# Kernel optimization log

Measured on AMD Instinct MI355X. Metric: run time of the kernel, lower is better.

Reference implementation:

```python
import jax, jax.numpy as jnp
import numpy as np

ALPHA = 0.1
BETA = 1.1
NUM_CLASSES = 16
EPS = 1e-8  # matches torch cosine_similarity eps
BATCH = 131072
DIM = 512


def setup_inputs() -> dict:
    key = jax.random.key(0)
    k1, k2 = jax.random.split(key)
    embeddings = jax.random.normal(k1, (BATCH, DIM), dtype=jnp.float32)
    labels = jax.random.randint(k2, (BATCH,), 0, NUM_CLASSES)
    return {"embeddings": embeddings, "labels": labels}


def _cos_dist(a, b):
    # a: [M, D], b: [N, D] -> 1 - cosine_similarity, shape [M, N]
    an = a / jnp.maximum(jnp.linalg.norm(a, axis=-1, keepdims=True), EPS)
    bn = b / jnp.maximum(jnp.linalg.norm(b, axis=-1, keepdims=True), EPS)
    return 1.0 - an @ bn.T


def reference(embeddings, labels):
    C = NUM_CLASSES
    N = embeddings.shape[0]
    dt = embeddings.dtype

    # class centroids (dummy anchors) via scatter-mean
    cnt = jax.ops.segment_sum(jnp.ones((N,), dt), labels, num_segments=C)  # [C]
    sums = jax.ops.segment_sum(embeddings, labels, num_segments=C)        # [C, D]
    centroids = sums / jnp.maximum(cnt, 1.0)[:, None]
    present = cnt > 0

    # close class pairs: i < j, both present, centroid distance <= beta
    pd = _cos_dist(centroids, centroids)                    # [C, C]
    upper = jnp.triu(jnp.ones((C, C), bool), k=1)
    pairmask = upper & (pd <= BETA) & present[:, None] & present[None, :]
    pm = pairmask.astype(dt)
    deg = pm.sum(1) + pm.sum(0)                             # pairs involving each class

    # distances from every centroid to every sample
    D = _cos_dist(centroids, embeddings)                    # [C, N]

    # intra: each sample of class c contributes relu(d(cent_c, x) - alpha),
    # once per close pair involving c
    d_own = D[labels, jnp.arange(N)]                        # [N]
    intra_sum = jnp.sum(deg[labels] * jax.nn.relu(d_own - ALPHA))

    # inter: S[c, c'] = sum over samples with label c' of relu(beta - d(cent_c, x))
    S = jax.ops.segment_sum(jax.nn.relu(BETA - D).T, labels, num_segments=C).T  # [C, C]
    inter_sum = jnp.sum(pm * (S + S.T))

    # number of terms in each loss list: sum over pairs of (cnt_i + cnt_j)
    count = jnp.sum(deg * cnt)
    denom = jnp.maximum(count, 1.0)
    num_pairs = pm.sum()

    loss = jnp.where(num_pairs > 0, intra_sum / denom + inter_sum / denom, 0.0)
    return loss
```

## Files before the change

### kernel.cpp

```cpp
#include <hip/hip_runtime.h>

constexpr float kAlpha = 0.1f;
constexpr float kBeta  = 1.1f;
constexpr int   kC     = 16;
constexpr int   kD     = 512;
constexpr float kEps   = 1e-8f;

constexpr int SUMS_OFF = 0;
constexpr int CNT_OFF  = 8192;
constexpr int TOT_OFF  = 8208;
constexpr int CN_OFF   = 8224;
constexpr int MSK_OFF  = 16416;
constexpr int SCL_OFF  = 16432;
constexpr int ZERO_FLOATS = 8209;

__device__ __forceinline__ float dot4(float4 a, float4 b) {
    return a.x * b.x + a.y * b.y + a.z * b.z + a.w * b.w;
}
__device__ __forceinline__ void add4(float4& a, float4 b) {
    a.x += b.x; a.y += b.y; a.z += b.z; a.w += b.w;
}

__global__ __launch_bounds__(256) void k1_sums(const float* __restrict__ emb,
                                               const int* __restrict__ labels,
                                               float* __restrict__ sums,
                                               float* __restrict__ cnt,
                                               int N, int rpb) {
    __shared__ float lacc[kC * kD];
    __shared__ float lcnt[kC];
    int tid = threadIdx.x;
    int wave = tid >> 6, lane = tid & 63;

    for (int i = tid; i < kC * kD; i += 256) lacc[i] = 0.f;
    if (tid < kC) lcnt[tid] = 0.f;

    float4 accA[kC], accB[kC];
#pragma unroll
    for (int c = 0; c < kC; ++c) {
        accA[c] = make_float4(0.f, 0.f, 0.f, 0.f);
        accB[c] = make_float4(0.f, 0.f, 0.f, 0.f);
    }
    float cacc = 0.f;

    const float4* e4 = (const float4*)emb;
    int r0 = blockIdx.x * rpb;
    int r1 = min(r0 + rpb, N);

#define ACC1(c) { add4(accA[c], a0); add4(accB[c], a1); }
#define DO_SWITCH(l)                                                        \
    switch (l) {                                                            \
        case 0:  ACC1(0);  break; case 1:  ACC1(1);  break;                 \
        case 2:  ACC1(2);  break; case 3:  ACC1(3);  break;                 \
        case 4:  ACC1(4);  break; case 5:  ACC1(5);  break;                 \
        case 6:  ACC1(6);  break; case 7:  ACC1(7);  break;                 \
        case 8:  ACC1(8);  break; case 9:  ACC1(9);  break;                 \
        case 10: ACC1(10); break; case 11: ACC1(11); break;                 \
        case 12: ACC1(12); break; case 13: ACC1(13); break;                 \
        case 14: ACC1(14); break; default: ACC1(15); break;                 \
    }

    int r = r0 + wave;
    bool v = (r < r1);
    int rc = v ? r : 0;
    float4 a0 = e4[(size_t)rc * 128 + lane];
    float4 a1 = e4[(size_t)rc * 128 + 64 + lane];
    int la = labels[rc];

    while (v) {
        int rn = r + 4;
        bool vn = (rn < r1);
        int rcn = vn ? rn : 0;
        float4 b0 = e4[(size_t)rcn * 128 + lane];
        float4 b1 = e4[(size_t)rcn * 128 + 64 + lane];
        int lb = labels[rcn];

        int l = __builtin_amdgcn_readfirstlane(la);
        DO_SWITCH(l);
        cacc += (lane < kC && l == lane) ? 1.f : 0.f;

        a0 = b0; a1 = b1; la = lb;
        r = rn; v = vn;
    }
#undef DO_SWITCH
#undef ACC1

    __syncthreads();
#pragma unroll
    for (int c = 0; c < kC; ++c) {
        float* pA = &lacc[c * kD + 4 * lane];
        atomicAdd(pA + 0, accA[c].x);
        atomicAdd(pA + 1, accA[c].y);
        atomicAdd(pA + 2, accA[c].z);
        atomicAdd(pA + 3, accA[c].w);
        float* pB = &lacc[c * kD + 256 + 4 * lane];
        atomicAdd(pB + 0, accB[c].x);
        atomicAdd(pB + 1, accB[c].y);
        atomicAdd(pB + 2, accB[c].z);
        atomicAdd(pB + 3, accB[c].w);
    }
    if (lane < kC) atomicAdd(&lcnt[lane], cacc);
    __syncthreads();
    for (int i = tid; i < kC * kD; i += 256) atomicAdd(&sums[i], lacc[i]);
    if (tid < kC) atomicAdd(&cnt[tid], lcnt[tid]);
}

__global__ __launch_bounds__(256) void k2_cent(const float* __restrict__ sums,
                                               const float* __restrict__ cnt_g,
                                               float* __restrict__ cn_g,
                                               unsigned* __restrict__ mask_g,
                                               float* __restrict__ scal) {
    __shared__ __align__(16) float lcn[kC * kD];
    __shared__ float lcnt[kC];
    __shared__ float red[256];
    __shared__ float norms[kC];
    __shared__ float pdm[kC * kC];
    int tid = threadIdx.x;
    if (tid < kC) lcnt[tid] = cnt_g[tid];
    __syncthreads();

    int c = tid >> 4, sub = tid & 15;
    float invc = 1.f / fmaxf(lcnt[c], 1.f);
    float sq = 0.f;
    for (int d = sub; d < kD; d += 16) {
        float v = sums[c * kD + d] * invc;
        lcn[c * kD + d] = v;
        sq += v * v;
    }
    red[tid] = sq;
    __syncthreads();
    if (tid < kC) {
        float t = 0.f;
        for (int k = 0; k < 16; ++k) t += red[tid * 16 + k];
        norms[tid] = fmaxf(sqrtf(t), kEps);
    }
    __syncthreads();
    for (int i = tid; i < kC * kD; i += 256) {
        float v = lcn[i] / norms[i / kD];
        lcn[i] = v;
        cn_g[i] = v;
    }
    __syncthreads();
    int pi = tid >> 4, pj = tid & 15;
    float dot = 0.f;
    for (int dd = 0; dd < kD; ++dd) {
        int d = (dd + tid) & (kD - 1);
        dot += lcn[pi * kD + d] * lcn[pj * kD + d];
    }
    pdm[tid] = 1.f - dot;
    __syncthreads();
    if (tid == 0) {
        unsigned m[kC];
        for (int a = 0; a < kC; ++a) m[a] = 0u;
        float npairs = 0.f;
        for (int a = 0; a < kC; ++a)
            for (int b = a + 1; b < kC; ++b) {
                bool close = (pdm[a * kC + b] <= kBeta) && (lcnt[a] > 0.f) && (lcnt[b] > 0.f);
                if (close) { m[a] |= 1u << b; m[b] |= 1u << a; npairs += 1.f; }
            }
        float count = 0.f;
        for (int a = 0; a < kC; ++a) {
            mask_g[a] = m[a];
            count += (float)__popc(m[a]) * lcnt[a];
        }
        scal[0] = fmaxf(count, 1.f);
        scal[1] = npairs;
    }
}

constexpr int TR = 32;
__global__ __launch_bounds__(512, 2) void k3_main(const float* __restrict__ emb,
                                                  const int* __restrict__ labels,
                                                  const float* __restrict__ cn_g,
                                                  const unsigned* __restrict__ mask_g,
                                                  float* __restrict__ total,
                                                  int N, int rpb) {
    __shared__ __align__(16) float4 xbuf[TR * 128];
    __shared__ unsigned lmask[kC];
    __shared__ float wsum[8];
    int tid = threadIdx.x;
    int wave = tid >> 6, lane = tid & 63;
    int g = lane >> 4, j = lane & 15;

    const float4* w4 = (const float4*)cn_g;
    float4 wreg[4][8];
#pragma unroll
    for (int c = 0; c < 4; ++c)
#pragma unroll
        for (int i = 0; i < 8; ++i)
            wreg[c][i] = w4[(4 * g + c) * 128 + i * 16 + j];
    if (tid < kC) lmask[tid] = mask_g[tid];

    int r0 = blockIdx.x * rpb;
    int r1 = min(r0 + rpb, N);
    float priv = 0.f;

    const float4* src = (const float4*)emb;
    float4 st[8];

    if (r0 < r1) {
        int avail = (r1 - r0) * 128;
#pragma unroll
        for (int k = 0; k < 8; ++k) {
            int idx = k * 512 + tid;
            st[k] = (idx < avail) ? src[(size_t)r0 * 128 + idx] : make_float4(0.f, 0.f, 0.f, 0.f);
        }
#pragma unroll
        for (int k = 0; k < 8; ++k) xbuf[k * 512 + tid] = st[k];
    }
    __syncthreads();

    for (int rt = r0; rt < r1; rt += TR) {
        int ntile = rt + TR;
        bool more = (ntile < r1);
        if (more) {
            int avail = (r1 - ntile) * 128;
#pragma unroll
            for (int k = 0; k < 8; ++k) {
                int idx = k * 512 + tid;
                st[k] = (idx < avail) ? src[(size_t)ntile * 128 + idx] : make_float4(0.f, 0.f, 0.f, 0.f);
            }
        }

        int rows = min(TR, r1 - rt);
        for (int rr = wave; rr < rows; rr += 8) {
            int row = rt + rr;
            int lab = labels[row];
            const float4* xr = &xbuf[rr * 128];
            float d0 = 0.f, d1 = 0.f, d2 = 0.f, d3 = 0.f, nrm = 0.f;
#pragma unroll
            for (int i = 0; i < 8; ++i) {
                float4 x = xr[i * 16 + j];
                nrm += dot4(x, x);
                d0 += dot4(x, wreg[0][i]);
                d1 += dot4(x, wreg[1][i]);
                d2 += dot4(x, wreg[2][i]);
                d3 += dot4(x, wreg[3][i]);
            }
#pragma unroll
            for (int m = 1; m < 16; m <<= 1) {
                d0 += __shfl_xor(d0, m, 64);
                d1 += __shfl_xor(d1, m, 64);
                d2 += __shfl_xor(d2, m, 64);
                d3 += __shfl_xor(d3, m, 64);
                nrm += __shfl_xor(nrm, m, 64);
            }
            if (j == 0) {
                unsigned mm = lmask[lab];
                float inv = 1.f / fmaxf(sqrtf(nrm), kEps);
                float s = 0.f;
                float dv[4] = {d0, d1, d2, d3};
#pragma unroll
                for (int c = 0; c < 4; ++c) {
                    int cg = 4 * g + c;
                    float dd = 1.f - dv[c] * inv;
                    if ((mm >> cg) & 1u) s += fmaxf(kBeta - dd, 0.f);
                    if (cg == lab) s += (float)__popc(mm) * fmaxf(dd - kAlpha, 0.f);
                }
                priv += s;
            }
        }
        __syncthreads();
        if (more) {
#pragma unroll
            for (int k = 0; k < 8; ++k) xbuf[k * 512 + tid] = st[k];
        }
        __syncthreads();
    }

#pragma unroll
    for (int off = 32; off > 0; off >>= 1) priv += __shfl_down(priv, off, 64);
    if (lane == 0) wsum[wave] = priv;
    __syncthreads();
    if (tid == 0) {
        float t = 0.f;
#pragma unroll
        for (int w = 0; w < 8; ++w) t += wsum[w];
        atomicAdd(total, t);
    }
}

__global__ void k4_final(const float* __restrict__ total,
                         const float* __restrict__ scal,
                         float* __restrict__ out) {
    out[0] = (scal[1] > 0.f) ? (total[0] / scal[0]) : 0.f;
}

extern "C" void kernel_launch(void* const* d_in, const int* in_sizes, int n_in,
                              void* d_out, int out_size, void* d_ws, size_t ws_size,
                              hipStream_t stream) {
    const float* emb = (const float*)d_in[0];
    const int* labels = (const int*)d_in[1];
    int N = in_sizes[0] / kD;

    float* ws = (float*)d_ws;
    float* sums = ws + SUMS_OFF;
    float* cnt = ws + CNT_OFF;
    float* total = ws + TOT_OFF;
    float* cn = ws + CN_OFF;
    unsigned* mask = (unsigned*)(ws + MSK_OFF);
    float* scal = ws + SCL_OFF;

    hipMemsetAsync(d_ws, 0, ZERO_FLOATS * sizeof(float), stream);

    int blocks1 = 512;
    int rpb1 = (N + blocks1 - 1) / blocks1;
    k1_sums<<<blocks1, 256, 0, stream>>>(emb, labels, sums, cnt, N, rpb1);

    k2_cent<<<1, 256, 0, stream>>>(sums, cnt, cn, mask, scal);

    int blocks3 = 256;
    int rpb3 = (N + blocks3 - 1) / blocks3;
    k3_main<<<blocks3, 512, 0, stream>>>(emb, labels, cn, mask, total, N, rpb3);

    k4_final<<<1, 1, 0, stream>>>(total, scal, (float*)d_out);
}
```

Measured before the change: 580.1 us.

## Stage k1 rows through shared memory, write per-block partials, and reshape k3 launch

The class-sum kernel now loads 16-row tiles cooperatively into shared memory with register prefetch. Each wave accumulates half a row's columns, and the block merges its results in LDS without shared atomics. When the workspace is large enough, each block writes its partial sums to global memory, and a new reduction kernel adds them instead of issuing global atomics per block. The main distance kernel goes from 256 blocks of 512 threads to 512 blocks of 256 threads with smaller tiles. The trade-off is an extra launch and about 16 MB of partial-buffer traffic, in exchange for removing atomic contention and getting more coalesced loads.

```diff
diff --git a/kernel.cpp b/kernel.cpp
--- a/kernel.cpp
+++ b/kernel.cpp
@@ -12,7 +12,9 @@
 constexpr int CN_OFF   = 8224;
 constexpr int MSK_OFF  = 16416;
 constexpr int SCL_OFF  = 16432;
+constexpr int PART_OFF = 16448;
 constexpr int ZERO_FLOATS = 8209;
+constexpr int PB = 512;
 
 __device__ __forceinline__ float dot4(float4 a, float4 b) {
     return a.x * b.x + a.y * b.y + a.z * b.z + a.w * b.w;
@@ -21,32 +23,30 @@
     a.x += b.x; a.y += b.y; a.z += b.z; a.w += b.w;
 }
 
-__global__ __launch_bounds__(256) void k1_sums(const float* __restrict__ emb,
-                                               const int* __restrict__ labels,
-                                               float* __restrict__ sums,
-                                               float* __restrict__ cnt,
-                                               int N, int rpb) {
-    __shared__ float lacc[kC * kD];
-    __shared__ float lcnt[kC];
+constexpr int T1R = 16;
+__global__ __launch_bounds__(256, 2) void k1_sums(const float* __restrict__ emb,
+                                                  const int* __restrict__ labels,
+                                                  float* __restrict__ partials,
+                                                  float* __restrict__ sums_direct,
+                                                  float* __restrict__ cnt,
+                                                  int N, int rpb, int use_partials) {
+    __shared__ __align__(16) float xbuf[T1R * kD];
     int tid = threadIdx.x;
     int wave = tid >> 6, lane = tid & 63;
-
-    for (int i = tid; i < kC * kD; i += 256) lacc[i] = 0.f;
-    if (tid < kC) lcnt[tid] = 0.f;
-
-    float4 accA[kC], accB[kC];
-#pragma unroll
-    for (int c = 0; c < kC; ++c) {
-        accA[c] = make_float4(0.f, 0.f, 0.f, 0.f);
-        accB[c] = make_float4(0.f, 0.f, 0.f, 0.f);
-    }
+    int rowPar = wave >> 1;
+    int half = wave & 1;
+
+    float4 acc[kC];
+#pragma unroll
+    for (int c = 0; c < kC; ++c) acc[c] = make_float4(0.f, 0.f, 0.f, 0.f);
     float cacc = 0.f;
 
-    const float4* e4 = (const float4*)emb;
     int r0 = blockIdx.x * rpb;
     int r1 = min(r0 + rpb, N);
-
-#define ACC1(c) { add4(accA[c], a0); add4(accB[c], a1); }
+    const float4* src = (const float4*)emb;
+    float4 st[8];
+
+#define ACC1(c) { add4(acc[c], x); }
 #define DO_SWITCH(l)                                                        \
     switch (l) {                                                            \
         case 0:  ACC1(0);  break; case 1:  ACC1(1);  break;                 \
@@ -59,49 +59,86 @@
         case 14: ACC1(14); break; default: ACC1(15); break;                 \
     }
 
-    int r = r0 + wave;
-    bool v = (r < r1);
-    int rc = v ? r : 0;
-    float4 a0 = e4[(size_t)rc * 128 + lane];
-    float4 a1 = e4[(size_t)rc * 128 + 64 + lane];
-    int la = labels[rc];
-
-    while (v) {
-        int rn = r + 4;
-        bool vn = (rn < r1);
-        int rcn = vn ? rn : 0;
-        float4 b0 = e4[(size_t)rcn * 128 + lane];
-        float4 b1 = e4[(size_t)rcn * 128 + 64 + lane];
-        int lb = labels[rcn];
-
-        int l = __builtin_amdgcn_readfirstlane(la);
-        DO_SWITCH(l);
-        cacc += (lane < kC && l == lane) ? 1.f : 0.f;
-
-        a0 = b0; a1 = b1; la = lb;
-        r = rn; v = vn;
+    if (r0 < r1) {
+        int avail = (r1 - r0) * 128;
+#pragma unroll
+        for (int k = 0; k < 8; ++k) {
+            int idx = k * 256 + tid;
+            st[k] = (idx < avail) ? src[(size_t)r0 * 128 + idx] : make_float4(0.f, 0.f, 0.f, 0.f);
+        }
+#pragma unroll
+        for (int k = 0; k < 8; ++k) ((float4*)xbuf)[k * 256 + tid] = st[k];
+    }
+    __syncthreads();
+
+    for (int rt = r0; rt < r1; rt += T1R) {
+        int ntile = rt + T1R;
+        bool more = (ntile < r1);
+        if (more) {
+            int avail = (r1 - ntile) * 128;
+#pragma unroll
+            for (int k = 0; k < 8; ++k) {
+                int idx = k * 256 + tid;
+                st[k] = (idx < avail) ? src[(size_t)ntile * 128 + idx] : make_float4(0.f, 0.f, 0.f, 0.f);
+            }
+        }
+
+        int rows = min(T1R, r1 - rt);
+        for (int rr = rowPar; rr < rows; rr += 2) {
+            int row = rt + rr;
+            int l = __builtin_amdgcn_readfirstlane(labels[row]);
+            float4 x = *(const float4*)&xbuf[rr * kD + half * 256 + lane * 4];
+            DO_SWITCH(l);
+            if (half == 0) cacc += (lane == l) ? 1.f : 0.f;
+        }
+        __syncthreads();
+        if (more) {
+#pragma unroll
+            for (int k = 0; k < 8; ++k) ((float4*)xbuf)[k * 256 + tid] = st[k];
+        }
+        __syncthreads();
     }
 #undef DO_SWITCH
 #undef ACC1
 
-    __syncthreads();
-#pragma unroll
-    for (int c = 0; c < kC; ++c) {
-        float* pA = &lacc[c * kD + 4 * lane];
-        atomicAdd(pA + 0, accA[c].x);
-        atomicAdd(pA + 1, accA[c].y);
-        atomicAdd(pA + 2, accA[c].z);
-        atomicAdd(pA + 3, accA[c].w);
-        float* pB = &lacc[c * kD + 256 + 4 * lane];
-        atomicAdd(pB + 0, accB[c].x);
-        atomicAdd(pB + 1, accB[c].y);
-        atomicAdd(pB + 2, accB[c].z);
-        atomicAdd(pB + 3, accB[c].w);
-    }
-    if (lane < kC) atomicAdd(&lcnt[lane], cacc);
-    __syncthreads();
-    for (int i = tid; i < kC * kD; i += 256) atomicAdd(&sums[i], lacc[i]);
-    if (tid < kC) atomicAdd(&cnt[tid], lcnt[tid]);
+    for (int i = tid; i < kC * kD; i += 256) xbuf[i] = 0.f;
+    __syncthreads();
+    if (rowPar == 0) {
+#pragma unroll
+        for (int c = 0; c < kC; ++c)
+            *(float4*)&xbuf[c * kD + half * 256 + lane * 4] = acc[c];
+    }
+    __syncthreads();
+    if (rowPar == 1) {
+#pragma unroll
+        for (int c = 0; c < kC; ++c) {
+            float4* p = (float4*)&xbuf[c * kD + half * 256 + lane * 4];
+            float4 t = *p;
+            add4(t, acc[c]);
+            *p = t;
+        }
+    }
+    __syncthreads();
+
+    if (use_partials) {
+        float4* dst = (float4*)(partials + (size_t)blockIdx.x * (kC * kD));
+#pragma unroll
+        for (int k = 0; k < 8; ++k) dst[k * 256 + tid] = ((float4*)xbuf)[k * 256 + tid];
+    } else {
+        for (int i = tid; i < kC * kD; i += 256) atomicAdd(&sums_direct[i], xbuf[i]);
+    }
+    if (half == 0 && lane < kC) atomicAdd(&cnt[lane], cacc);
+}
+
+__global__ __launch_bounds__(256) void k1b_reduce(const float* __restrict__ partials,
+                                                  float* __restrict__ sums) {
+    int col = blockIdx.x * 256 + threadIdx.x;
+    int rBeg = blockIdx.y * (PB / 16);
+    float s = 0.f;
+#pragma unroll 8
+    for (int r = rBeg; r < rBeg + PB / 16; ++r)
+        s += partials[(size_t)r * (kC * kD) + col];
+    atomicAdd(&sums[col], s);
 }
 
 __global__ __launch_bounds__(256) void k2_cent(const float* __restrict__ sums,
@@ -167,16 +204,16 @@
     }
 }
 
-constexpr int TR = 32;
-__global__ __launch_bounds__(512, 2) void k3_main(const float* __restrict__ emb,
+constexpr int T3R = 16;
+__global__ __launch_bounds__(256, 2) void k3_main(const float* __restrict__ emb,
                                                   const int* __restrict__ labels,
                                                   const float* __restrict__ cn_g,
                                                   const unsigned* __restrict__ mask_g,
                                                   float* __restrict__ total,
                                                   int N, int rpb) {
-    __shared__ __align__(16) float4 xbuf[TR * 128];
+    __shared__ __align__(16) float4 xbuf[T3R * 128];
     __shared__ unsigned lmask[kC];
-    __shared__ float wsum[8];
+    __shared__ float wsum[4];
     int tid = threadIdx.x;
     int wave = tid >> 6, lane = tid & 63;
     int g = lane >> 4, j = lane & 15;
@@ -201,28 +238,28 @@
         int avail = (r1 - r0) * 128;
 #pragma unroll
         for (int k = 0; k < 8; ++k) {
-            int idx = k * 512 + tid;
+            int idx = k * 256 + tid;
             st[k] = (idx < avail) ? src[(size_t)r0 * 128 + idx] : make_float4(0.f, 0.f, 0.f, 0.f);
         }
 #pragma unroll
-        for (int k = 0; k < 8; ++k) xbuf[k * 512 + tid] = st[k];
-    }
-    __syncthreads();
-
-    for (int rt = r0; rt < r1; rt += TR) {
-        int ntile = rt + TR;
+        for (int k = 0; k < 8; ++k) xbuf[k * 256 + tid] = st[k];
+    }
+    __syncthreads();
+
+    for (int rt = r0; rt < r1; rt += T3R) {
+        int ntile = rt + T3R;
         bool more = (ntile < r1);
         if (more) {
             int avail = (r1 - ntile) * 128;
 #pragma unroll
             for (int k = 0; k < 8; ++k) {
-                int idx = k * 512 + tid;
+                int idx = k * 256 + tid;
                 st[k] = (idx < avail) ? src[(size_t)ntile * 128 + idx] : make_float4(0.f, 0.f, 0.f, 0.f);
             }
         }
 
-        int rows = min(TR, r1 - rt);
-        for (int rr = wave; rr < rows; rr += 8) {
+        int rows = min(T3R, r1 - rt);
+        for (int rr = wave; rr < rows; rr += 4) {
             int row = rt + rr;
             int lab = labels[row];
             const float4* xr = &xbuf[rr * 128];
@@ -262,7 +299,7 @@
         __syncthreads();
         if (more) {
 #pragma unroll
-            for (int k = 0; k < 8; ++k) xbuf[k * 512 + tid] = st[k];
+            for (int k = 0; k < 8; ++k) xbuf[k * 256 + tid] = st[k];
         }
         __syncthreads();
     }
@@ -271,12 +308,7 @@
     for (int off = 32; off > 0; off >>= 1) priv += __shfl_down(priv, off, 64);
     if (lane == 0) wsum[wave] = priv;
     __syncthreads();
-    if (tid == 0) {
-        float t = 0.f;
-#pragma unroll
-        for (int w = 0; w < 8; ++w) t += wsum[w];
-        atomicAdd(total, t);
-    }
+    if (tid == 0) atomicAdd(total, wsum[0] + wsum[1] + wsum[2] + wsum[3]);
 }
 
 __global__ void k4_final(const float* __restrict__ total,
@@ -299,18 +331,24 @@
     float* cn = ws + CN_OFF;
     unsigned* mask = (unsigned*)(ws + MSK_OFF);
     float* scal = ws + SCL_OFF;
+    float* partials = ws + PART_OFF;
+
+    size_t need = ((size_t)PART_OFF + (size_t)PB * kC * kD) * sizeof(float);
+    int use_partials = (ws_size >= need) ? 1 : 0;
 
     hipMemsetAsync(d_ws, 0, ZERO_FLOATS * sizeof(float), stream);
 
-    int blocks1 = 512;
-    int rpb1 = (N + blocks1 - 1) / blocks1;
-    k1_sums<<<blocks1, 256, 0, stream>>>(emb, labels, sums, cnt, N, rpb1);
+    int rpb1 = (N + PB - 1) / PB;
+    k1_sums<<<PB, 256, 0, stream>>>(emb, labels, partials, sums, cnt, N, rpb1, use_partials);
+
+    if (use_partials)
+        k1b_reduce<<<dim3(32, 16), 256, 0, stream>>>(partials, sums);
 
     k2_cent<<<1, 256, 0, stream>>>(sums, cnt, cn, mask, scal);
 
-    int blocks3 = 256;
+    int blocks3 = 512;
     int rpb3 = (N + blocks3 - 1) / blocks3;
-    k3_main<<<blocks3, 512, 0, stream>>>(emb, labels, cn, mask, total, N, rpb3);
+    k3_main<<<blocks3, 256, 0, stream>>>(emb, labels, cn, mask, total, N, rpb3);
 
     k4_final<<<1, 1, 0, stream>>>(total, scal, (float*)d_out);
 }
```

New measurement: 586.0 us. About the same (+1.0%).
